# Performance work log

Measured on AMD Instinct MI355X. Metric: run time of the kernel, lower is better.

Reference implementation:

```python
import jax, jax.numpy as jnp
import numpy as np

IMG = 64
N = IMG * IMG          # 4096, spatial tokens = LayerNorm dim
F2 = 128 * 128         # 16384, feature_size**2 = Mlp input dim
B, C = 8, 512
EPS = 1e-5
LOG_MAX = float(np.log(1.0 / 0.01))  # clamp max for logit_scale


def setup_inputs() -> dict:
    key = jax.random.key(0)
    ks = jax.random.split(key, 8)
    s1 = 1.0 / np.sqrt(F2)
    s2 = 1.0 / np.sqrt(N)
    return {
        "x": jax.random.normal(ks[0], (B, C, N), jnp.float32),
        "feature": jax.random.normal(ks[1], (B, C, F2), jnp.float32),
        "fc1_w": jax.random.uniform(ks[2], (N, F2), jnp.float32, -s1, s1),
        "fc1_b": jax.random.uniform(ks[3], (N,), jnp.float32, -s1, s1),
        "fc2_w": jax.random.uniform(ks[4], (N, N), jnp.float32, -s2, s2),
        "fc2_b": jax.random.uniform(ks[5], (N,), jnp.float32, -s2, s2),
        "logit_scale": jnp.full((1, 1, N), np.log(10.0), jnp.float32),
        "norm_w": jnp.ones((N,), jnp.float32),
        "norm_b": jnp.zeros((N,), jnp.float32),
    }


def reference(x, feature, fc1_w, fc1_b, fc2_w, fc2_b, logit_scale, norm_w, norm_b):
    # Mlp: (B,C,F2) -> (B,C,N), ReLU activation, drop=0
    h = jax.nn.relu(jnp.einsum('bcf,nf->bcn', feature, fc1_w) + fc1_b)
    feat = jnp.einsum('bch,nh->bcn', h, fc2_w) + fc2_b        # (B,C,N)
    feat = jnp.swapaxes(feat, 1, 2)                            # (B,N,C)
    scale = jnp.exp(jnp.minimum(logit_scale, LOG_MAX))         # (1,1,N)
    temp = jnp.einsum('bnc,bcm->bnm', feat, x) * scale         # (B,N,N)
    temp = jax.nn.softmax(temp, axis=1)                        # softmax over dim=1
    out = jnp.einsum('bcn,bnm->bcm', x, temp)                  # (B,C,N)
    # LayerNorm over last dim
    mu = jnp.mean(out, axis=-1, keepdims=True)
    var = jnp.var(out, axis=-1, keepdims=True)
    out = (out - mu) * jax.lax.rsqrt(var + EPS) * norm_w + norm_b
    return out
```

## Files before the change

kernel.cpp:

```cpp
#include <hip/hip_runtime.h>
#include <stdint.h>

using u16 = unsigned short;
typedef unsigned int u32;
typedef __attribute__((ext_vector_type(4))) float f32x4;
typedef __attribute__((ext_vector_type(8))) short short8;

typedef const __attribute__((address_space(1))) u32* gas_ptr;
typedef __attribute__((address_space(3))) u32* las_ptr;

__device__ __forceinline__ u16 f2bf_u(float f) {
    u32 u = __builtin_bit_cast(u32, f);
    u32 r = 0x7fffu + ((u >> 16) & 1u);
    return (u16)((u + r) >> 16);
}
__device__ __forceinline__ float bfu2f(u16 h) {
    u32 u = ((u32)h) << 16;
    return __builtin_bit_cast(float, u);
}
__device__ __forceinline__ void split2(float v, u16& hi, u16& lo) {
    hi = f2bf_u(v);
    lo = f2bf_u(v - bfu2f(hi));
}

__device__ __forceinline__ void gload16(const void* g, void* l) {
    __builtin_amdgcn_global_load_lds((gas_ptr)g, (las_ptr)l, 16, 0, 0);
}

template<int EPI, bool SPLIT>
__global__ __launch_bounds__(512, 2)
void gemm256(const u16* __restrict__ Ah, const u16* __restrict__ Al,
             const u16* __restrict__ Bh, const u16* __restrict__ Bl,
             int K, int lda, int N,
             const float* __restrict__ aux,
             void* __restrict__ out0, void* __restrict__ out1,
             size_t strideA, size_t strideB, size_t strideO)
{
    extern __shared__ __align__(16) u16 lds[];
    u16* const As0 = lds;
    u16* const Bs0 = lds + 16384;
    u16* const As1 = lds + 32768;
    u16* const Bs1 = lds + 49152;

    const int t = threadIdx.x;
    const int w = t >> 6;
    const int l = t & 63;

    int brow, bcol;
    const int gx = gridDim.x, gy = gridDim.y;
    const int orig = blockIdx.y * gx + blockIdx.x;
    if (gx == 16 && gy == 16) {
        const int x = orig & 7, j = orig >> 3;
        brow = ((x & 3) * 4 + (j & 3)) * 256;
        bcol = ((x >> 2) * 8 + (j >> 2)) * 256;
    } else {
        const int nwg = gx * gy;
        const int swz = (orig & 7) * (nwg >> 3) + (orig >> 3);
        brow = (swz / gx) * 256;
        bcol = (swz % gx) * 256;
    }
    const int z = blockIdx.z;

    const u16* A0 = Ah + (size_t)z * strideA;
    const u16* A1 = SPLIT ? (Al + (size_t)z * strideA) : nullptr;
    const u16* B0 = Bh + (size_t)z * strideB;
    const u16* B1 = SPLIT ? (Bl + (size_t)z * strideB) : nullptr;

    const int srow = l >> 2;
    const int sca = ((l & 3) ^ ((l >> 3) & 3)) * 8;

    const int wr = w >> 2;
    const int wc = w & 3;
    const int lr = l & 15;
    const int cr = ((l >> 4) ^ ((l >> 1) & 3)) * 8;

    f32x4 acc[8][4];
    const f32x4 zero = {0.f, 0.f, 0.f, 0.f};
#pragma unroll
    for (int i = 0; i < 8; ++i)
#pragma unroll
        for (int j = 0; j < 4; ++j) acc[i][j] = zero;

    const int NT = K >> 5;

    auto STAGE = [&](int buf, int kt) {
        const int kk = kt << 5;
#pragma unroll
        for (int it = 0; it < 2; ++it) {
            const int rbase = it * 128 + w * 16;
            const int lo = buf * 8192 + rbase * 32;
            const size_t ga = (size_t)(brow + rbase + srow) * lda + (kk + sca);
            const size_t gb = (size_t)(bcol + rbase + srow) * lda + (kk + sca);
            gload16(A0 + ga, &As0[lo]);
            gload16(B0 + gb, &Bs0[lo]);
            if constexpr (SPLIT) {
                gload16(A1 + ga, &As1[lo]);
                gload16(B1 + gb, &Bs1[lo]);
            }
        }
    };

    STAGE(0, 0);
    __syncthreads();
    int cur = 0;

    for (int kt = 0; kt < NT; ++kt) {
        if (kt + 1 < NT) STAGE(cur ^ 1, kt + 1);
        short8 bh[4], bl[4];
#pragma unroll
        for (int n = 0; n < 4; ++n) {
            const int ro = cur * 8192 + (wc * 64 + n * 16 + lr) * 32 + cr;
            bh[n] = *(const short8*)&Bs0[ro];
            if constexpr (SPLIT) bl[n] = *(const short8*)&Bs1[ro];
        }
#pragma unroll
        for (int mh = 0; mh < 2; ++mh) {
            short8 ah[4], al[4];
#pragma unroll
            for (int m = 0; m < 4; ++m) {
                const int ro = cur * 8192 + (wr * 128 + mh * 64 + m * 16 + lr) * 32 + cr;
                ah[m] = *(const short8*)&As0[ro];
                if constexpr (SPLIT) al[m] = *(const short8*)&As1[ro];
            }
            __builtin_amdgcn_s_setprio(1);
#pragma unroll
            for (int m = 0; m < 4; ++m)
#pragma unroll
                for (int n = 0; n < 4; ++n)
                    acc[mh * 4 + m][n] = __builtin_amdgcn_mfma_f32_16x16x32_bf16(
                        ah[m], bh[n], acc[mh * 4 + m][n], 0, 0, 0);
            if constexpr (SPLIT) {
#pragma unroll
                for (int m = 0; m < 4; ++m)
#pragma unroll
                    for (int n = 0; n < 4; ++n)
                        acc[mh * 4 + m][n] = __builtin_amdgcn_mfma_f32_16x16x32_bf16(
                            al[m], bh[n], acc[mh * 4 + m][n], 0, 0, 0);
#pragma unroll
                for (int m = 0; m < 4; ++m)
#pragma unroll
                    for (int n = 0; n < 4; ++n)
                        acc[mh * 4 + m][n] = __builtin_amdgcn_mfma_f32_16x16x32_bf16(
                            ah[m], bl[n], acc[mh * 4 + m][n], 0, 0, 0);
            }
            __builtin_amdgcn_s_setprio(0);
        }
        __syncthreads();
        cur ^= 1;
    }

#pragma unroll
    for (int mh = 0; mh < 2; ++mh)
#pragma unroll
        for (int m = 0; m < 4; ++m)
#pragma unroll
            for (int n = 0; n < 4; ++n)
#pragma unroll
                for (int j = 0; j < 4; ++j) {
                    const int row = brow + wr * 128 + mh * 64 + m * 16 + (l >> 4) * 4 + j;
                    const int col = bcol + wc * 64 + n * 16 + (l & 15);
                    float v = acc[mh * 4 + m][n][j];
                    if (EPI == 0) {
                        v += aux[col];
                        v = fmaxf(v, 0.f);
                        u16 hi, lo; split2(v, hi, lo);
                        ((u16*)out0)[(size_t)row * N + col] = hi;
                        ((u16*)out1)[(size_t)row * N + col] = lo;
                    } else if (EPI == 1) {
                        v += aux[col];
                        const int bb = row >> 9, cc = row & 511;
                        const size_t idx = ((size_t)bb * N + col) * 512 + cc;
                        u16 hi, lo; split2(v, hi, lo);
                        ((u16*)out0)[idx] = hi;
                        ((u16*)out1)[idx] = lo;
                    } else if (EPI == 2) {
                        ((float*)out0)[(size_t)row * N + col] = v;
                    } else {
                        ((float*)out0)[(size_t)z * strideO + (size_t)row * N + col] = v;
                    }
                }
}

__global__ void split_k(const float* __restrict__ in, u16* __restrict__ hi,
                        u16* __restrict__ lo, size_t n4)
{
    size_t i = blockIdx.x * (size_t)blockDim.x + threadIdx.x;
    const size_t stride = (size_t)gridDim.x * blockDim.x;
    for (; i < n4; i += stride) {
        const float4 v = ((const float4*)in)[i];
        ushort4 h, l;
        split2(v.x, h.x, l.x);
        split2(v.y, h.y, l.y);
        split2(v.z, h.z, l.z);
        split2(v.w, h.w, l.w);
        ((ushort4*)hi)[i] = h;
        ((ushort4*)lo)[i] = l;
    }
}

__global__ void conv_bf16_k(const float* __restrict__ in, u16* __restrict__ out, size_t n4)
{
    size_t i = blockIdx.x * (size_t)blockDim.x + threadIdx.x;
    const size_t stride = (size_t)gridDim.x * blockDim.x;
    for (; i < n4; i += stride) {
        const float4 v = ((const float4*)in)[i];
        ushort4 o;
        o.x = f2bf_u(v.x); o.y = f2bf_u(v.y); o.z = f2bf_u(v.z); o.w = f2bf_u(v.w);
        ((ushort4*)out)[i] = o;
    }
}

__global__ void transpose_split_x(const float* __restrict__ x,
                                  u16* __restrict__ xt_hi, u16* __restrict__ xt_lo)
{
    __shared__ float tile[32][33];
    const int b = blockIdx.z;
    const int n0 = blockIdx.x * 32;
    const int c0 = blockIdx.y * 32;
    const int tx = threadIdx.x, ty = threadIdx.y;
#pragma unroll
    for (int k = 0; k < 4; ++k)
        tile[ty + 8 * k][tx] = x[((size_t)b * 512 + c0 + ty + 8 * k) * 4096 + n0 + tx];
    __syncthreads();
#pragma unroll
    for (int k = 0; k < 4; ++k) {
        const float v = tile[tx][ty + 8 * k];
        u16 hi, lo; split2(v, hi, lo);
        const size_t idx = ((size_t)b * 4096 + n0 + ty + 8 * k) * 512 + c0 + tx;
        xt_hi[idx] = hi;
        xt_lo[idx] = lo;
    }
}

__global__ void scale_prep(const float* __restrict__ ls, float* __restrict__ s)
{
    const int i = blockIdx.x * blockDim.x + threadIdx.x;
    if (i < 4096) s[i] = expf(fminf(ls[i], 4.605170185988092f));
}

__global__ __launch_bounds__(256)
void softmax_rows(const float* __restrict__ T, const float* __restrict__ s, u16* __restrict__ P)
{
    const int m = blockIdx.x;
    const int t = threadIdx.x;
    const float sc = s[m];
    const float* row = T + (size_t)m * 4096;
    float v[16];
    float mx = -3.402823e38f;
#pragma unroll
    for (int i = 0; i < 16; ++i) {
        v[i] = row[t + 256 * i] * sc;
        mx = fmaxf(mx, v[i]);
    }
#pragma unroll
    for (int o = 32; o; o >>= 1) mx = fmaxf(mx, __shfl_xor(mx, o, 64));
    __shared__ float sm[4], ss[4];
    if ((t & 63) == 0) sm[t >> 6] = mx;
    __syncthreads();
    mx = fmaxf(fmaxf(sm[0], sm[1]), fmaxf(sm[2], sm[3]));
    float sum = 0.f;
#pragma unroll
    for (int i = 0; i < 16; ++i) {
        v[i] = expf(v[i] - mx);
        sum += v[i];
    }
#pragma unroll
    for (int o = 32; o; o >>= 1) sum += __shfl_xor(sum, o, 64);
    if ((t & 63) == 0) ss[t >> 6] = sum;
    __syncthreads();
    sum = (ss[0] + ss[1]) + (ss[2] + ss[3]);
    const float inv = 1.f / sum;
#pragma unroll
    for (int i = 0; i < 16; ++i)
        P[(size_t)m * 4096 + t + 256 * i] = f2bf_u(v[i] * inv);
}

__global__ __launch_bounds__(256)
void ln_rows(const float* __restrict__ X, const float* __restrict__ gw,
             const float* __restrict__ gb, float* __restrict__ out)
{
    const int r = blockIdx.x;
    const int t = threadIdx.x;
    const float* row = X + (size_t)r * 4096;
    float v[16];
    float s1 = 0.f, s2 = 0.f;
#pragma unroll
    for (int i = 0; i < 16; ++i) {
        v[i] = row[t + 256 * i];
        s1 += v[i];
        s2 += v[i] * v[i];
    }
#pragma unroll
    for (int o = 32; o; o >>= 1) {
        s1 += __shfl_xor(s1, o, 64);
        s2 += __shfl_xor(s2, o, 64);
    }
    __shared__ float m1[4], m2[4];
    if ((t & 63) == 0) { m1[t >> 6] = s1; m2[t >> 6] = s2; }
    __syncthreads();
    s1 = (m1[0] + m1[1]) + (m1[2] + m1[3]);
    s2 = (m2[0] + m2[1]) + (m2[2] + m2[3]);
    const float mu = s1 * (1.f / 4096.f);
    const float var = s2 * (1.f / 4096.f) - mu * mu;
    const float rs = rsqrtf(var + 1e-5f);
#pragma unroll
    for (int i = 0; i < 16; ++i) {
        const int n = t + 256 * i;
        out[(size_t)r * 4096 + n] = (v[i] - mu) * rs * gw[n] + gb[n];
    }
}

extern "C" void kernel_launch(void* const* d_in, const int* in_sizes, int n_in,
                              void* d_out, int out_size, void* d_ws, size_t ws_size,
                              hipStream_t stream)
{
    const float* x  = (const float*)d_in[0];
    const float* fe = (const float*)d_in[1];
    const float* w1 = (const float*)d_in[2];
    const float* b1 = (const float*)d_in[3];
    const float* w2 = (const float*)d_in[4];
    const float* b2 = (const float*)d_in[5];
    const float* ls = (const float*)d_in[6];
    const float* nw = (const float*)d_in[7];
    const float* nb = (const float*)d_in[8];
    float* out = (float*)d_out;
    char* ws = (char*)d_ws;

    if (ws_size < 637550592ull) return;

    static_assert(sizeof(void*) == 8, "");
    hipFuncSetAttribute((const void*)gemm256<0, true>,
                        hipFuncAttributeMaxDynamicSharedMemorySize, 131072);
    hipFuncSetAttribute((const void*)gemm256<1, true>,
                        hipFuncAttributeMaxDynamicSharedMemorySize, 131072);
    hipFuncSetAttribute((const void*)gemm256<2, true>,
                        hipFuncAttributeMaxDynamicSharedMemorySize, 131072);

    u16*  fhi  = (u16*) (ws + 0ull);
    u16*  flo  = (u16*) (ws + 134217728ull);
    u16*  w1hi = (u16*) (ws + 268435456ull);
    u16*  w1lo = (u16*) (ws + 402653184ull);
    u16*  hhi  = (u16*) (ws + 536870912ull);
    u16*  hlo  = (u16*) (ws + 570425344ull);
    u16*  w2hi = (u16*) (ws + 0ull);
    u16*  w2lo = (u16*) (ws + 33554432ull);
    u16*  fthi = (u16*) (ws + 67108864ull);
    u16*  ftlo = (u16*) (ws + 100663296ull);
    u16*  xthi = (u16*) (ws + 134217728ull);
    u16*  xtlo = (u16*) (ws + 167772160ull);
    u16*  xbf  = (u16*) (ws + 201326592ull);
    float* tt  = (float*)(ws + 234881024ull);
    u16*  pall = (u16*) (ws + 301989888ull);
    float* pre = (float*)(ws + 570425344ull);
    float* sv  = (float*)(ws + 637534208ull);

    split_k<<<2048, 256, 0, stream>>>(fe, fhi, flo, (size_t)16777216);
    split_k<<<2048, 256, 0, stream>>>(w1, w1hi, w1lo, (size_t)16777216);

    gemm256<0, true><<<dim3(16, 16, 1), 512, 131072, stream>>>(
        fhi, flo, w1hi, w1lo, 16384, 16384, 4096, b1, hhi, hlo, 0, 0, 0);

    split_k<<<2048, 256, 0, stream>>>(w2, w2hi, w2lo, (size_t)4194304);

    gemm256<1, true><<<dim3(16, 16, 1), 512, 131072, stream>>>(
        hhi, hlo, w2hi, w2lo, 4096, 4096, 4096, b2, fthi, ftlo, 0, 0, 0);

    transpose_split_x<<<dim3(128, 16, 8), dim3(32, 8), 0, stream>>>(x, xthi, xtlo);
    conv_bf16_k<<<2048, 256, 0, stream>>>(x, xbf, (size_t)4194304);
    scale_prep<<<16, 256, 0, stream>>>(ls, sv);

    for (int b = 0; b < 8; ++b) {
        const size_t o = (size_t)b * 4096 * 512;
        gemm256<2, true><<<dim3(16, 16, 1), 512, 131072, stream>>>(
            xthi + o, xtlo + o, fthi + o, ftlo + o, 512, 512, 4096,
            nullptr, tt, nullptr, 0, 0, 0);
        softmax_rows<<<4096, 256, 0, stream>>>(tt, sv, pall + (size_t)b * 16777216);
    }

    gemm256<3, false><<<dim3(16, 2, 8), 512, 65536, stream>>>(
        xbf, nullptr, pall, nullptr, 4096, 4096, 4096, nullptr, pre, nullptr,
        (size_t)512 * 4096, (size_t)4096 * 4096, (size_t)512 * 4096);

    ln_rows<<<4096, 256, 0, stream>>>(pre, nw, nb, out);
}
```

Baseline: 2.703 ms.

## Triple-buffer LDS pipeline and load B-low fragments directly from global into registers

Replaces the double-buffered GEMM main loop with a three-stage LDS ring that prefetches two K-tiles ahead. Waits now use explicit vmcnt counts and a raw barrier instead of a full __syncthreads. The B low-part operand no longer goes through LDS; it is loaded straight from global memory into registers two tiles ahead, saving LDS space and staging traffic. LDS per block rises from 128KB to 144KB, which likely drops occupancy to one block per CU. The direct global loads are uncoalesced per-lane 16-byte reads, and the hand-counted vmcnt values could be fragile.

```diff
diff --git a/kernel.cpp b/kernel.cpp
--- a/kernel.cpp
+++ b/kernel.cpp
@@ -26,6 +26,90 @@
 __device__ __forceinline__ void gload16(const void* g, void* l) {
     __builtin_amdgcn_global_load_lds((gas_ptr)g, (las_ptr)l, 16, 0, 0);
 }
+
+
+#define STAGE(CBUF, KT)                                                      \
+  {                                                                          \
+    const int kk_ = (KT) << 5;                                               \
+    _Pragma("unroll")                                                        \
+    for (int it_ = 0; it_ < 2; ++it_) {                                      \
+      const int rb_ = it_ * 128 + w * 16;                                    \
+      const int lo_ = (CBUF) * 8192 + rb_ * 32;                              \
+      const size_t ga_ = (size_t)(brow + rb_ + srow) * lda + (kk_ + sca);    \
+      const size_t gb_ = (size_t)(bcol + rb_ + srow) * lda + (kk_ + sca);    \
+      gload16(A0 + ga_, &As0[lo_]);                                          \
+      gload16(B0 + gb_, &Bs0[lo_]);                                          \
+      if constexpr (SPLIT) gload16(A1 + ga_, &As1[lo_]);                     \
+    }                                                                        \
+  }
+
+#define BLOQ(Q, KT)                                                          \
+  {                                                                          \
+    const u16* bb_ = B1 + (size_t)(bcol + wc * 64 + lr) * lda                \
+                     + (((KT) << 5) + ((l >> 4) * 8));                       \
+    _Pragma("unroll")                                                        \
+    for (int n_ = 0; n_ < 4; ++n_)                                           \
+      Q[n_] = *(const short8*)(bb_ + (size_t)(n_ * 16) * lda);               \
+  }
+
+#define PHASE(KT, CBUF, Q)                                                   \
+  {                                                                          \
+    if ((KT) == NT - 1) {                                                    \
+      asm volatile("s_waitcnt vmcnt(0)" ::: "memory");                       \
+    } else {                                                                 \
+      if constexpr (SPLIT) asm volatile("s_waitcnt vmcnt(10)" ::: "memory"); \
+      else asm volatile("s_waitcnt vmcnt(4)" ::: "memory");                  \
+    }                                                                        \
+    __builtin_amdgcn_s_barrier();                                            \
+    __builtin_amdgcn_sched_barrier(0);                                       \
+    {                                                                        \
+      int cs_ = (CBUF) + 2; if (cs_ >= 3) cs_ -= 3;                          \
+      if ((KT) + 2 < NT) STAGE(cs_, (KT) + 2);                               \
+    }                                                                        \
+    short8 bh_[4];                                                           \
+    _Pragma("unroll")                                                        \
+    for (int n_ = 0; n_ < 4; ++n_)                                           \
+      bh_[n_] = *(const short8*)&Bs0[(CBUF) * 8192 +                         \
+                                     (wc * 64 + n_ * 16 + lr) * 32 + cr];    \
+    _Pragma("unroll")                                                        \
+    for (int mh_ = 0; mh_ < 2; ++mh_) {                                      \
+      short8 ah_[4], al_[4];                                                 \
+      _Pragma("unroll")                                                      \
+      for (int m_ = 0; m_ < 4; ++m_) {                                       \
+        const int ro_ = (CBUF) * 8192 +                                      \
+                        (wr * 128 + mh_ * 64 + m_ * 16 + lr) * 32 + cr;      \
+        ah_[m_] = *(const short8*)&As0[ro_];                                 \
+        if constexpr (SPLIT) al_[m_] = *(const short8*)&As1[ro_];            \
+      }                                                                      \
+      __builtin_amdgcn_s_setprio(1);                                         \
+      _Pragma("unroll")                                                      \
+      for (int m_ = 0; m_ < 4; ++m_)                                         \
+        _Pragma("unroll")                                                    \
+        for (int n_ = 0; n_ < 4; ++n_)                                       \
+          acc[mh_ * 4 + m_][n_] = __builtin_amdgcn_mfma_f32_16x16x32_bf16(   \
+              ah_[m_], bh_[n_], acc[mh_ * 4 + m_][n_], 0, 0, 0);             \
+      if constexpr (SPLIT) {                                                 \
+        _Pragma("unroll")                                                    \
+        for (int m_ = 0; m_ < 4; ++m_)                                       \
+          _Pragma("unroll")                                                  \
+          for (int n_ = 0; n_ < 4; ++n_)                                     \
+            acc[mh_ * 4 + m_][n_] = __builtin_amdgcn_mfma_f32_16x16x32_bf16( \
+                al_[m_], bh_[n_], acc[mh_ * 4 + m_][n_], 0, 0, 0);           \
+        _Pragma("unroll")                                                    \
+        for (int m_ = 0; m_ < 4; ++m_)                                       \
+          _Pragma("unroll")                                                  \
+          for (int n_ = 0; n_ < 4; ++n_)                                     \
+            acc[mh_ * 4 + m_][n_] = __builtin_amdgcn_mfma_f32_16x16x32_bf16( \
+                ah_[m_], Q[n_], acc[mh_ * 4 + m_][n_], 0, 0, 0);             \
+      }                                                                      \
+      __builtin_amdgcn_s_setprio(0);                                         \
+    }                                                                        \
+    __builtin_amdgcn_sched_barrier(0);                                       \
+    if ((KT) + 2 < NT) {                                                     \
+      if constexpr (SPLIT) BLOQ(Q, (KT) + 2);                                \
+    }                                                                        \
+    __builtin_amdgcn_sched_barrier(0);                                       \
+  }
 
 template<int EPI, bool SPLIT>
 __global__ __launch_bounds__(512, 2)
@@ -38,9 +122,8 @@
 {
     extern __shared__ __align__(16) u16 lds[];
     u16* const As0 = lds;
-    u16* const Bs0 = lds + 16384;
-    u16* const As1 = lds + 32768;
-    u16* const Bs1 = lds + 49152;
+    u16* const Bs0 = lds + 3 * 8192;
+    u16* const As1 = SPLIT ? (lds + 6 * 8192) : lds;
 
     const int t = threadIdx.x;
     const int w = t >> 6;
@@ -82,71 +165,19 @@
         for (int j = 0; j < 4; ++j) acc[i][j] = zero;
 
     const int NT = K >> 5;
-
-    auto STAGE = [&](int buf, int kt) {
-        const int kk = kt << 5;
-#pragma unroll
-        for (int it = 0; it < 2; ++it) {
-            const int rbase = it * 128 + w * 16;
-            const int lo = buf * 8192 + rbase * 32;
-            const size_t ga = (size_t)(brow + rbase + srow) * lda + (kk + sca);
-            const size_t gb = (size_t)(bcol + rbase + srow) * lda + (kk + sca);
-            gload16(A0 + ga, &As0[lo]);
-            gload16(B0 + gb, &Bs0[lo]);
-            if constexpr (SPLIT) {
-                gload16(A1 + ga, &As1[lo]);
-                gload16(B1 + gb, &Bs1[lo]);
-            }
-        }
-    };
+    short8 qA[4], qB[4];
 
     STAGE(0, 0);
-    __syncthreads();
-    int cur = 0;
-
-    for (int kt = 0; kt < NT; ++kt) {
-        if (kt + 1 < NT) STAGE(cur ^ 1, kt + 1);
-        short8 bh[4], bl[4];
-#pragma unroll
-        for (int n = 0; n < 4; ++n) {
-            const int ro = cur * 8192 + (wc * 64 + n * 16 + lr) * 32 + cr;
-            bh[n] = *(const short8*)&Bs0[ro];
-            if constexpr (SPLIT) bl[n] = *(const short8*)&Bs1[ro];
-        }
-#pragma unroll
-        for (int mh = 0; mh < 2; ++mh) {
-            short8 ah[4], al[4];
-#pragma unroll
-            for (int m = 0; m < 4; ++m) {
-                const int ro = cur * 8192 + (wr * 128 + mh * 64 + m * 16 + lr) * 32 + cr;
-                ah[m] = *(const short8*)&As0[ro];
-                if constexpr (SPLIT) al[m] = *(const short8*)&As1[ro];
-            }
-            __builtin_amdgcn_s_setprio(1);
-#pragma unroll
-            for (int m = 0; m < 4; ++m)
-#pragma unroll
-                for (int n = 0; n < 4; ++n)
-                    acc[mh * 4 + m][n] = __builtin_amdgcn_mfma_f32_16x16x32_bf16(
-                        ah[m], bh[n], acc[mh * 4 + m][n], 0, 0, 0);
-            if constexpr (SPLIT) {
-#pragma unroll
-                for (int m = 0; m < 4; ++m)
-#pragma unroll
-                    for (int n = 0; n < 4; ++n)
-                        acc[mh * 4 + m][n] = __builtin_amdgcn_mfma_f32_16x16x32_bf16(
-                            al[m], bh[n], acc[mh * 4 + m][n], 0, 0, 0);
-#pragma unroll
-                for (int m = 0; m < 4; ++m)
-#pragma unroll
-                    for (int n = 0; n < 4; ++n)
-                        acc[mh * 4 + m][n] = __builtin_amdgcn_mfma_f32_16x16x32_bf16(
-                            ah[m], bl[n], acc[mh * 4 + m][n], 0, 0, 0);
-            }
-            __builtin_amdgcn_s_setprio(0);
-        }
-        __syncthreads();
-        cur ^= 1;
+    if constexpr (SPLIT) BLOQ(qA, 0);
+    STAGE(1, 1);
+    if constexpr (SPLIT) BLOQ(qB, 1);
+
+    int c = 0;
+    for (int kt = 0; kt < NT; kt += 2) {
+        PHASE(kt, c, qA);
+        c = (c == 2) ? 0 : c + 1;
+        PHASE(kt + 1, c, qB);
+        c = (c == 2) ? 0 : c + 1;
     }
 
 #pragma unroll
@@ -328,13 +359,14 @@
 
     if (ws_size < 637550592ull) return;
 
-    static_assert(sizeof(void*) == 8, "");
     hipFuncSetAttribute((const void*)gemm256<0, true>,
-                        hipFuncAttributeMaxDynamicSharedMemorySize, 131072);
+                        hipFuncAttributeMaxDynamicSharedMemorySize, 147456);
     hipFuncSetAttribute((const void*)gemm256<1, true>,
-                        hipFuncAttributeMaxDynamicSharedMemorySize, 131072);
+                        hipFuncAttributeMaxDynamicSharedMemorySize, 147456);
     hipFuncSetAttribute((const void*)gemm256<2, true>,
-                        hipFuncAttributeMaxDynamicSharedMemorySize, 131072);
+                        hipFuncAttributeMaxDynamicSharedMemorySize, 147456);
+    hipFuncSetAttribute((const void*)gemm256<3, false>,
+                        hipFuncAttributeMaxDynamicSharedMemorySize, 98304);
 
     u16*  fhi  = (u16*) (ws + 0ull);
     u16*  flo  = (u16*) (ws + 134217728ull);
@@ -357,12 +389,12 @@
     split_k<<<2048, 256, 0, stream>>>(fe, fhi, flo, (size_t)16777216);
     split_k<<<2048, 256, 0, stream>>>(w1, w1hi, w1lo, (size_t)16777216);
 
-    gemm256<0, true><<<dim3(16, 16, 1), 512, 131072, stream>>>(
+    gemm256<0, true><<<dim3(16, 16, 1), 512, 147456, stream>>>(
         fhi, flo, w1hi, w1lo, 16384, 16384, 4096, b1, hhi, hlo, 0, 0, 0);
 
     split_k<<<2048, 256, 0, stream>>>(w2, w2hi, w2lo, (size_t)4194304);
 
-    gemm256<1, true><<<dim3(16, 16, 1), 512, 131072, stream>>>(
+    gemm256<1, true><<<dim3(16, 16, 1), 512, 147456, stream>>>(
         hhi, hlo, w2hi, w2lo, 4096, 4096, 4096, b2, fthi, ftlo, 0, 0, 0);
 
     transpose_split_x<<<dim3(128, 16, 8), dim3(32, 8), 0, stream>>>(x, xthi, xtlo);
@@ -371,13 +403,13 @@
 
     for (int b = 0; b < 8; ++b) {
         const size_t o = (size_t)b * 4096 * 512;
-        gemm256<2, true><<<dim3(16, 16, 1), 512, 131072, stream>>>(
+        gemm256<2, true><<<dim3(16, 16, 1), 512, 147456, stream>>>(
             xthi + o, xtlo + o, fthi + o, ftlo + o, 512, 512, 4096,
             nullptr, tt, nullptr, 0, 0, 0);
         softmax_rows<<<4096, 256, 0, stream>>>(tt, sv, pall + (size_t)b * 16777216);
     }
 
-    gemm256<3, false><<<dim3(16, 2, 8), 512, 65536, stream>>>(
+    gemm256<3, false><<<dim3(16, 2, 8), 512, 98304, stream>>>(
         xbf, nullptr, pall, nullptr, 4096, 4096, 4096, nullptr, pre, nullptr,
         (size_t)512 * 4096, (size_t)4096 * 4096, (size_t)512 * 4096);
 
```

After: 2.691 ms. Within noise of the previous version (-0.5%).
